# Optimization experiments

Measured on AMD Instinct MI355X. Metric: run time of the kernel, lower is better.

Reference implementation:

```python
import jax, jax.numpy as jnp
import numpy as np
from jax import lax

B, T_IN, T_OUT = 64, 200, 400
D_ENC, D_ARNN, D_DRNN = 512, 1024, 1024
PRENET, ATT_DIM, NFILT, KSIZE, NMEL = 256, 128, 32, 31, 80


def setup_inputs() -> dict:
    key = jax.random.key(0)
    ks = jax.random.split(key, 20)
    sc = lambda k, shape: (jax.random.normal(k, shape, jnp.float32) * 0.02)
    lengths = jnp.maximum(jax.random.randint(ks[0], (B,), 0, T_IN), T_IN // 2)
    return {
        'encoder_outputs': jax.random.normal(ks[1], (B, T_IN, D_ENC), jnp.float32),
        'decoder_inputs': jax.random.normal(ks[2], (T_OUT, B, NMEL), jnp.float32),
        'encoder_outputs_lengths': lengths,
        'W_p1': sc(ks[3], (PRENET, NMEL)),
        'W_p2': sc(ks[4], (PRENET, PRENET)),
        'W_ih_a': sc(ks[5], (4 * D_ARNN, PRENET + D_ENC)),
        'W_hh_a': sc(ks[6], (4 * D_ARNN, D_ARNN)),
        'b_a': jnp.zeros((4 * D_ARNN,), jnp.float32),
        'Wq': sc(ks[7], (ATT_DIM, D_ARNN)),
        'Wmem': sc(ks[8], (ATT_DIM, D_ENC)),
        'v': sc(ks[9], (ATT_DIM,)),
        'Wconv': sc(ks[10], (NFILT, 2, KSIZE)),
        'Wloc': sc(ks[11], (ATT_DIM, NFILT)),
        'W_ih_d': sc(ks[12], (4 * D_DRNN, D_ARNN + D_ENC)),
        'W_hh_d': sc(ks[13], (4 * D_DRNN, D_DRNN)),
        'b_d': jnp.zeros((4 * D_DRNN,), jnp.float32),
        'Wp': sc(ks[14], (NMEL, D_DRNN + D_ENC)),
        'bp': jnp.zeros((NMEL,), jnp.float32),
    }


def _lstm_cell(x, h, c, Wih, Whh, b):
    g = x @ Wih.T + h @ Whh.T + b
    i, f, gg, o = jnp.split(g, 4, axis=-1)
    c_new = jax.nn.sigmoid(f) * c + jax.nn.sigmoid(i) * jnp.tanh(gg)
    h_new = jax.nn.sigmoid(o) * jnp.tanh(c_new)
    return h_new, c_new


def reference(encoder_outputs, decoder_inputs, encoder_outputs_lengths,
              W_p1, W_p2, W_ih_a, W_hh_a, b_a, Wq, Wmem, v, Wconv, Wloc,
              W_ih_d, W_hh_d, b_d, Wp, bp):
    Bsz, T_in, _ = encoder_outputs.shape
    T_steps = decoder_inputs.shape[0]
    NEG = jnp.float32(-1e8)
    pad = (KSIZE - 1) // 2

    # go frame + prenet (prenet_dropout = 0.0 => pure relu MLP)
    go = jnp.zeros((1, Bsz, NMEL), decoder_inputs.dtype)
    di = jnp.concatenate([go, decoder_inputs], axis=0)          # [T+1, B, 80]
    pre = jax.nn.relu(jax.nn.relu(di @ W_p1.T) @ W_p2.T)        # [T+1, B, 256]
    xs = pre[:T_steps]                                          # step i uses pre[i]

    processed_memory = encoder_outputs @ Wmem.T                 # [B, T_in, att]
    mask = jnp.arange(T_in)[None, :] >= encoder_outputs_lengths[:, None]

    def step(carry, x_t):
        ah, ac, dh, dc, aw, aw_cum, actx = carry
        cell_in = jnp.concatenate([x_t, actx], axis=-1)
        ah, ac = _lstm_cell(cell_in, ah, ac, W_ih_a, W_hh_a, b_a)
        # location-sensitive attention
        awc = jnp.stack([aw, aw_cum], axis=1)                   # [B, 2, T_in]
        loc = lax.conv_general_dilated(awc, Wconv, (1,), [(pad, pad)],
                                       dimension_numbers=('NCH', 'OIH', 'NCH'))
        loc = jnp.swapaxes(loc, 1, 2) @ Wloc.T                  # [B, T_in, att]
        pq = (ah @ Wq.T)[:, None, :]                            # [B, 1, att]
        energies = jnp.tanh(pq + loc + processed_memory) @ v    # [B, T_in]
        energies = jnp.where(mask, NEG, energies)
        aw = jax.nn.softmax(energies, axis=1)
        actx = jnp.einsum('bt,bte->be', aw, encoder_outputs)
        aw_cum = aw_cum + aw
        dec_in = jnp.concatenate([ah, actx], axis=-1)
        dh, dc = _lstm_cell(dec_in, dh, dc, W_ih_d, W_hh_d, b_d)
        out = jnp.concatenate([dh, actx], axis=-1) @ Wp.T + bp  # [B, 80]
        return (ah, ac, dh, dc, aw, aw_cum, actx), (out, aw)

    z = lambda d: jnp.zeros((Bsz, d), encoder_outputs.dtype)
    carry0 = (z(D_ARNN), z(D_ARNN), z(D_DRNN), z(D_DRNN), z(T_in), z(T_in), z(D_ENC))
    _, (outs, aligns) = lax.scan(step, carry0, xs)
    return jnp.swapaxes(outs, 0, 1), jnp.swapaxes(aligns, 0, 1)  # [B,T,80], [B,T,T_in]
```

## Files before the change

kernel.cpp:

```cpp
#include <hip/hip_runtime.h>
#include <cstddef>
#include <cstdint>

#define T_INN 200
#define T_OUTT 400
#define BB 64
#define DENC 512
#define NMEL 80

typedef unsigned short u16;
typedef __bf16 bf16x8 __attribute__((ext_vector_type(8)));
typedef float f32x4 __attribute__((ext_vector_type(4)));
typedef float f32x2 __attribute__((ext_vector_type(2)));

__device__ __forceinline__ f32x2 pkfma(f32x2 a, f32x2 b, f32x2 c) {
  return __builtin_elementwise_fma(a, b, c);
}

__device__ __forceinline__ float sigf(float x) {
  return __builtin_amdgcn_rcpf(1.0f + __expf(-x));
}
__device__ __forceinline__ float ftanh(float x) {
  float e2 = __expf(2.0f * x);
  return 1.0f - 2.0f * __builtin_amdgcn_rcpf(e2 + 1.0f);
}

__device__ __forceinline__ u16 f2bf(float f) {
  unsigned u = __float_as_uint(f);
  unsigned r = u + 0x7fffu + ((u >> 16) & 1u);
  return (u16)(r >> 16);
}

__device__ __forceinline__ bf16x8 ldbf8(const u16* p) { return *(const bf16x8*)p; }

__global__ __launch_bounds__(256) void gemm_pre_kernel(
    const float* __restrict__ A, int lda, const float* __restrict__ W, int ldw,
    float* __restrict__ C, u16* __restrict__ Cbf, int ldc, int K, int relu)
{
  __shared__ float As[16][66];
  __shared__ float Ws[16][66];
  const int tid = threadIdx.x;
  const int tn = tid & 15, tm = tid >> 4;
  const int n0 = blockIdx.x * 64;
  const int m0 = blockIdx.y * 64;
  float acc[4][4] = {{0.f}};
  for (int kt = 0; kt < K; kt += 16) {
#pragma unroll
    for (int i = 0; i < 4; i++) {
      int e = tid + 256 * i;
      int m = e >> 4, kk = e & 15;
      As[kk][m] = A[(size_t)(m0 + m) * lda + kt + kk];
    }
#pragma unroll
    for (int i = 0; i < 4; i++) {
      int e = tid + 256 * i;
      int n = e >> 4, kk = e & 15;
      Ws[kk][n] = W[(size_t)(n0 + n) * ldw + kt + kk];
    }
    __syncthreads();
#pragma unroll
    for (int kk = 0; kk < 16; kk++) {
      float2 a01 = *(const float2*)&As[kk][tm * 4];
      float2 a23 = *(const float2*)&As[kk][tm * 4 + 2];
      float2 w01 = *(const float2*)&Ws[kk][tn * 4];
      float2 w23 = *(const float2*)&Ws[kk][tn * 4 + 2];
      float a[4] = {a01.x, a01.y, a23.x, a23.y};
      float w[4] = {w01.x, w01.y, w23.x, w23.y};
#pragma unroll
      for (int mi = 0; mi < 4; mi++)
#pragma unroll
        for (int ni = 0; ni < 4; ni++)
          acc[mi][ni] = fmaf(a[mi], w[ni], acc[mi][ni]);
    }
    __syncthreads();
  }
#pragma unroll
  for (int mi = 0; mi < 4; mi++) {
    int m = m0 + tm * 4 + mi;
    float v0 = acc[mi][0], v1 = acc[mi][1], v2 = acc[mi][2], v3 = acc[mi][3];
    if (relu) {
      v0 = fmaxf(v0, 0.f); v1 = fmaxf(v1, 0.f);
      v2 = fmaxf(v2, 0.f); v3 = fmaxf(v3, 0.f);
    }
    if (Cbf) {
      u16* p = Cbf + (size_t)m * ldc + n0 + tn * 4;
      p[0] = f2bf(v0); p[1] = f2bf(v1); p[2] = f2bf(v2); p[3] = f2bf(v3);
    } else {
      float4 vv; vv.x = v0; vv.y = v1; vv.z = v2; vv.w = v3;
      *(float4*)&C[(size_t)m * ldc + n0 + tn * 4] = vv;
    }
  }
}

__global__ __launch_bounds__(256) void pack_w_kernel(
    const float* __restrict__ W, u16* __restrict__ P,
    int K, int KTl, int ktOff, int KTtot, int total)
{
  int slot = blockIdx.x * 256 + threadIdx.x;
  if (slot >= total) return;
  int lane = slot & 63;
  int ktl = (slot >> 6) % KTl;
  int nt = slot / (64 * KTl);
  int n = nt * 16 + (lane & 15);
  int k = ktl * 32 + (lane >> 4) * 8;
  const float* src = W + (size_t)n * K + k;
  u16 tmp[8];
#pragma unroll
  for (int i = 0; i < 8; i++) tmp[i] = f2bf(src[i]);
  u16* dst = P + ((size_t)(nt * KTtot + (ktl + ktOff)) * 64 + lane) * 8;
  *(uint4*)dst = *(const uint4*)tmp;
}

__global__ void transpose_pm_kernel(const float* __restrict__ pm, float* __restrict__ pmT)
{
  int b = blockIdx.z;
  int tT = blockIdx.x * 32, aT = blockIdx.y * 32;
  __shared__ float tile[32][33];
  int tx = threadIdx.x, ty = threadIdx.y;
#pragma unroll
  for (int i = 0; i < 4; i++) {
    int t = tT + ty + i * 8;
    int a = aT + tx;
    if (t < T_INN) tile[ty + i * 8][tx] = pm[((size_t)b * T_INN + t) * 128 + a];
  }
  __syncthreads();
#pragma unroll
  for (int i = 0; i < 4; i++) {
    int a = aT + ty + i * 8;
    int t = tT + tx;
    if (t < T_INN) pmT[((size_t)b * 128 + a) * T_INN + t] = tile[tx][ty + i * 8];
  }
}

struct SmemGates {
  float part[16][16][66];
  float gred[1024];
};

__global__ __launch_bounds__(1024, 4) void gates_kernel(
    const u16* __restrict__ xs,
    const u16* __restrict__ actx_bf,
    const u16* __restrict__ ah_bf_r, u16* __restrict__ ah_bf_w,
    const u16* __restrict__ dh_bf_r, u16* __restrict__ dh_bf_w,
    const u16* __restrict__ Wa, const u16* __restrict__ Wd,
    const float* __restrict__ b_a, const float* __restrict__ b_d,
    float* __restrict__ ah, float* __restrict__ ac,
    float* __restrict__ dh, float* __restrict__ dc, int t)
{
  const int z = blockIdx.z;
  if (z == 0 && t >= T_OUTT) return;
  if (z == 1 && t < 1) return;
  const int bq = blockIdx.x, ms2 = blockIdx.y;
  const int tid = threadIdx.x;
  const int kw = tid >> 6, lane = tid & 63;
  const int mrow = lane & 15, ksub = (lane >> 4) * 8;
  const int rowL = ms2 * 32 + mrow;
  const int rowH = rowL + 16;
  __shared__ SmemGates sg;

  f32x4 zero4 = {0.f, 0.f, 0.f, 0.f};
  f32x4 aL0 = zero4, aL1 = zero4, aL2 = zero4, aL3 = zero4;
  f32x4 aH0 = zero4, aH1 = zero4, aH2 = zero4, aH3 = zero4;
  const float* bias; float* hF; float* cSt; u16* hw;

  if (z == 0) {
    constexpr int KT = 64;
    const size_t gstride = (size_t)KT * 32768;
    const u16* wb0 = Wa + ((size_t)(bq * KT + kw * 4) * 64 + lane) * 8;
    const u16* rbL; const u16* rbH;
    if (kw < 2) {
      rbL = xs + (size_t)rowL * 256 + ksub + kw * 128;
      rbH = xs + (size_t)rowH * 256 + ksub + kw * 128;
    } else if (kw < 6) {
      rbL = actx_bf + (size_t)rowL * 512 + ksub + kw * 128 - 256;
      rbH = actx_bf + (size_t)rowH * 512 + ksub + kw * 128 - 256;
    } else {
      rbL = ah_bf_r + (size_t)rowL * 1024 + ksub + kw * 128 - 768;
      rbH = ah_bf_r + (size_t)rowH * 1024 + ksub + kw * 128 - 768;
    }
#pragma unroll
    for (int i = 0; i < 4; i++) {
      bf16x8 al = ldbf8(rbL + i * 32);
      bf16x8 ahi = ldbf8(rbH + i * 32);
      const u16* wb = wb0 + (size_t)i * 512;
      bf16x8 w0 = ldbf8(wb);
      bf16x8 w1 = ldbf8(wb + gstride);
      bf16x8 w2 = ldbf8(wb + 2 * gstride);
      bf16x8 w3 = ldbf8(wb + 3 * gstride);
      aL0 = __builtin_amdgcn_mfma_f32_16x16x32_bf16(al, w0, aL0, 0, 0, 0);
      aL1 = __builtin_amdgcn_mfma_f32_16x16x32_bf16(al, w1, aL1, 0, 0, 0);
      aL2 = __builtin_amdgcn_mfma_f32_16x16x32_bf16(al, w2, aL2, 0, 0, 0);
      aL3 = __builtin_amdgcn_mfma_f32_16x16x32_bf16(al, w3, aL3, 0, 0, 0);
      aH0 = __builtin_amdgcn_mfma_f32_16x16x32_bf16(ahi, w0, aH0, 0, 0, 0);
      aH1 = __builtin_amdgcn_mfma_f32_16x16x32_bf16(ahi, w1, aH1, 0, 0, 0);
      aH2 = __builtin_amdgcn_mfma_f32_16x16x32_bf16(ahi, w2, aH2, 0, 0, 0);
      aH3 = __builtin_amdgcn_mfma_f32_16x16x32_bf16(ahi, w3, aH3, 0, 0, 0);
    }
    bias = b_a; hF = ah; cSt = ac; hw = ah_bf_w;
  } else {
    constexpr int KT = 80;
    const size_t gstride = (size_t)KT * 32768;
    const u16* wb0 = Wd + ((size_t)(bq * KT + kw) * 64 + lane) * 8;
    const u16* a0L = ah_bf_r + (size_t)rowL * 1024 + ksub + kw * 32;
    const u16* a1L = actx_bf + (size_t)rowL * 512  + ksub + kw * 32;
    const u16* a2L = dh_bf_r + (size_t)rowL * 1024 + ksub + kw * 32;
    const u16* a0H = ah_bf_r + (size_t)rowH * 1024 + ksub + kw * 32;
    const u16* a1H = actx_bf + (size_t)rowH * 512  + ksub + kw * 32;
    const u16* a2H = dh_bf_r + (size_t)rowH * 1024 + ksub + kw * 32;
#pragma unroll
    for (int i = 0; i < 5; i++) {
      const u16* apL = (i < 2) ? (a0L + i * 512) : ((i == 2) ? a1L : (a2L + (i - 3) * 512));
      const u16* apH = (i < 2) ? (a0H + i * 512) : ((i == 2) ? a1H : (a2H + (i - 3) * 512));
      bf16x8 al = ldbf8(apL);
      bf16x8 ahi = ldbf8(apH);
      const u16* wb = wb0 + (size_t)i * (16 * 512);
      bf16x8 w0 = ldbf8(wb);
      bf16x8 w1 = ldbf8(wb + gstride);
      bf16x8 w2 = ldbf8(wb + 2 * gstride);
      bf16x8 w3 = ldbf8(wb + 3 * gstride);
      aL0 = __builtin_amdgcn_mfma_f32_16x16x32_bf16(al, w0, aL0, 0, 0, 0);
      aL1 = __builtin_amdgcn_mfma_f32_16x16x32_bf16(al, w1, aL1, 0, 0, 0);
      aL2 = __builtin_amdgcn_mfma_f32_16x16x32_bf16(al, w2, aL2, 0, 0, 0);
      aL3 = __builtin_amdgcn_mfma_f32_16x16x32_bf16(al, w3, aL3, 0, 0, 0);
      aH0 = __builtin_amdgcn_mfma_f32_16x16x32_bf16(ahi, w0, aH0, 0, 0, 0);
      aH1 = __builtin_amdgcn_mfma_f32_16x16x32_bf16(ahi, w1, aH1, 0, 0, 0);
      aH2 = __builtin_amdgcn_mfma_f32_16x16x32_bf16(ahi, w2, aH2, 0, 0, 0);
      aH3 = __builtin_amdgcn_mfma_f32_16x16x32_bf16(ahi, w3, aH3, 0, 0, 0);
    }
    bias = b_d; hF = dh; cSt = dc; hw = dh_bf_w;
  }

#pragma unroll
  for (int h = 0; h < 2; h++) {
    if (h == 1) __syncthreads();
#pragma unroll
    for (int r = 0; r < 4; r++) {
      if (h == 0) {
        sg.part[kw][r][lane]      = aL0[r];
        sg.part[kw][4 + r][lane]  = aL1[r];
        sg.part[kw][8 + r][lane]  = aL2[r];
        sg.part[kw][12 + r][lane] = aL3[r];
      } else {
        sg.part[kw][r][lane]      = aH0[r];
        sg.part[kw][4 + r][lane]  = aH1[r];
        sg.part[kw][8 + r][lane]  = aH2[r];
        sg.part[kw][12 + r][lane] = aH3[r];
      }
    }
    __syncthreads();
    {
      int g = tid >> 8, rc = tid & 255, rw = rc >> 4, col = rc & 15;
      int ln = ((rw >> 2) << 4) + col;
      int r = g * 4 + (rw & 3);
      float s = 0.f;
#pragma unroll
      for (int k2 = 0; k2 < 16; k2++) s += sg.part[k2][r][ln];
      sg.gred[tid] = s;
    }
    __syncthreads();
    if (tid < 256) {
      int rw = tid >> 4, col = tid & 15;
      int j = bq * 16 + col, m = ms2 * 32 + h * 16 + rw;
      size_t idx = (size_t)m * 1024 + j;
      float gi = sg.gred[tid]       + bias[j];
      float gf = sg.gred[256 + tid] + bias[j + 1024];
      float gg = sg.gred[512 + tid] + bias[j + 2048];
      float go = sg.gred[768 + tid] + bias[j + 3072];
      float cn = sigf(gf) * cSt[idx] + sigf(gi) * ftanh(gg);
      cSt[idx] = cn;
      float hn = sigf(go) * ftanh(cn);
      hF[idx] = hn;
      hw[idx] = f2bf(hn);
    }
  }
}

__global__ __launch_bounds__(1024, 4) void fused_step_kernel(
    const float* __restrict__ ah, const float* __restrict__ dh,
    float* __restrict__ actx , u16* __restrict__ actx_bf,
    float* __restrict__ aw, float* __restrict__ awcum,
    const float* __restrict__ pmT, const float* __restrict__ Wq,
    const float* __restrict__ Wconv, const float* __restrict__ Wloc,
    const float* __restrict__ vvec, const int* __restrict__ lens,
    const float* __restrict__ enc, const float* __restrict__ Wp,
    const float* __restrict__ bp,
    float* __restrict__ outsOut, float* __restrict__ alignsOut, int t)
{
  const int tid = threadIdx.x;

  if (blockIdx.x >= 64) {
    if (t < 1) return;
    const int bo = blockIdx.x - 64;
    const float* actxR = actx + (size_t)((t - 1) & 1) * 32768;
    __shared__ float cp[1024];
    float s = 0.f;
    int m = tid / 12, sub = tid - m * 12;
    if (tid < 960) {
      const float4* w4 = (const float4*)(Wp + (size_t)m * 1536 + sub * 128);
      const float4* a4 = (sub < 8)
          ? (const float4*)(dh + (size_t)bo * 1024 + sub * 128)
          : (const float4*)(actxR + (size_t)bo * 512 + (sub - 8) * 128);
      f32x2 s2 = {0.f, 0.f};
#pragma unroll 8
      for (int kk = 0; kk < 32; kk++) {
        float4 w = w4[kk], av = a4[kk];
        s2 = pkfma(f32x2{w.x, w.y}, f32x2{av.x, av.y}, s2);
        s2 = pkfma(f32x2{w.z, w.w}, f32x2{av.z, av.w}, s2);
      }
      s = s2.x + s2.y;
    }
    cp[tid] = s;
    __syncthreads();
    if (tid < 80) {
      float acc2 = bp[tid];
#pragma unroll
      for (int i2 = 0; i2 < 12; i2++) acc2 += cp[tid * 12 + i2];
      outsOut[((size_t)bo * T_OUTT + (t - 1)) * NMEL + tid] = acc2;
    }
    return;
  }

  if (t >= T_OUTT) return;
  const int b = blockIdx.x;
  const int g = tid >> 8, ti = tid & 255;
  float* actxW = actx + (size_t)(t & 1) * 32768;

  __shared__ float2 acS[T_INN];
  __shared__ float ahS[1024];
  __shared__ float pp[128][9];
  __shared__ float pqS[128];
  __shared__ float convS[T_INN][33];
  __shared__ float ep[4][256];
  __shared__ float red[256];
  __shared__ float awS[256];
  __shared__ float cpart[1024];

  if (tid < T_INN) {
    float2 v; v.x = aw[b * T_INN + tid]; v.y = awcum[b * T_INN + tid];
    acS[tid] = v;
  }
  ahS[tid] = ah[(size_t)b * 1024 + tid];
  __syncthreads();
  {
    int a = tid >> 3, kc = tid & 7;
    const float4* wv = (const float4*)(Wq + (size_t)a * 1024 + kc * 128);
    const float4* hv = (const float4*)(ahS + kc * 128);
    f32x2 s2 = {0.f, 0.f};
#pragma unroll 8
    for (int i = 0; i < 32; i++) {
      float4 wq = wv[i], hh = hv[i];
      s2 = pkfma(f32x2{wq.x, wq.y}, f32x2{hh.x, hh.y}, s2);
      s2 = pkfma(f32x2{wq.z, wq.w}, f32x2{hh.z, hh.w}, s2);
    }
    pp[a][kc] = s2.x + s2.y;
  }
  __syncthreads();
  if (tid < 128) {
    float s = 0.f;
#pragma unroll
    for (int kc = 0; kc < 8; kc++) s += pp[tid][kc];
    pqS[tid] = s;
  }
  if (ti < T_INN) {
    f32x2 s2[4] = {{0.f, 0.f}, {0.f, 0.f}, {0.f, 0.f}, {0.f, 0.f}};
#pragma unroll
    for (int k = 0; k < 31; k++) {
      int tt = ti + k - 15;
      if (tt >= 0 && tt < T_INN) {
        float2 v = acS[tt];
        f32x2 vx = {v.x, v.x}, vy = {v.y, v.y};
#pragma unroll
        for (int p = 0; p < 4; p++) {
          int f = g * 8 + 2 * p;
          f32x2 wa = {Wconv[f * 62 + k],      Wconv[(f + 1) * 62 + k]};
          f32x2 wc = {Wconv[f * 62 + 31 + k], Wconv[(f + 1) * 62 + 31 + k]};
          s2[p] = pkfma(wa, vx, s2[p]);
          s2[p] = pkfma(wc, vy, s2[p]);
        }
      }
    }
#pragma unroll
    for (int p = 0; p < 4; p++) {
      convS[ti][g * 8 + 2 * p]     = s2[p].x;
      convS[ti][g * 8 + 2 * p + 1] = s2[p].y;
    }
  }
  __syncthreads();
  float e = 0.f;
  if (ti < T_INN) {
    float cv[32];
#pragma unroll
    for (int f = 0; f < 32; f++) cv[f] = convS[ti][f];
    const float* pm = pmT + ((size_t)b * 128 + g * 32) * T_INN + ti;
#pragma unroll 4
    for (int aa = 0; aa < 32; aa++) {
      int a = g * 32 + aa;
      const float* wl = Wloc + a * 32;
      f32x2 x2 = {0.f, 0.f};
#pragma unroll
      for (int j = 0; j < 16; j++) {
        f32x2 w2 = *(const f32x2*)&wl[2 * j];
        x2 = pkfma(w2, f32x2{cv[2 * j], cv[2 * j + 1]}, x2);
      }
      float x = pqS[a] + pm[(size_t)aa * T_INN] + x2.x + x2.y;
      float ex2 = __expf(2.f * x);
      e += vvec[a] * (1.f - 2.f * __builtin_amdgcn_rcpf(ex2 + 1.f));
    }
  }
  ep[g][ti] = e;
  __syncthreads();
  float ev = -3.0e38f, ex = 0.f;
  if (tid < 256) {
    if (tid < T_INN) {
      ev = ep[0][tid] + ep[1][tid] + ep[2][tid] + ep[3][tid];
      if (tid >= lens[b]) ev = -100000000.0f;
    }
    red[tid] = ev;
  }
  __syncthreads();
  for (int s2 = 128; s2 > 0; s2 >>= 1) {
    if (tid < s2) red[tid] = fmaxf(red[tid], red[tid + s2]);
    __syncthreads();
  }
  float mx = red[0];
  __syncthreads();
  if (tid < 256) { ex = (tid < T_INN) ? __expf(ev - mx) : 0.f; red[tid] = ex; }
  __syncthreads();
  for (int s2 = 128; s2 > 0; s2 >>= 1) {
    if (tid < s2) red[tid] += red[tid + s2];
    __syncthreads();
  }
  float inv = 1.0f / red[0];
  if (tid < T_INN) {
    float a = ex * inv;
    awS[tid] = a;
    aw[b * T_INN + tid] = a;
    awcum[b * T_INN + tid] = acS[tid].y + a;
    alignsOut[((size_t)b * T_OUTT + t) * T_INN + tid] = a;
  }
  __syncthreads();
  {
    int e0 = tid & 511, half = tid >> 9;
    const float* ep2 = enc + ((size_t)b * T_INN + half * 100) * DENC + e0;
    float s = 0.f;
#pragma unroll 4
    for (int tt = 0; tt < 100; tt++) s += awS[half * 100 + tt] * ep2[(size_t)tt * DENC];
    cpart[tid] = s;
  }
  __syncthreads();
  if (tid < 512) {
    float v2 = cpart[tid] + cpart[512 + tid];
    actxW[b * DENC + tid] = v2;
    actx_bf[b * DENC + tid] = f2bf(v2);
  }
}

extern "C" void kernel_launch(void* const* d_in, const int* in_sizes, int n_in,
                              void* d_out, int out_size, void* d_ws, size_t ws_size,
                              hipStream_t stream)
{
  const float* enc    = (const float*)d_in[0];
  const float* dec    = (const float*)d_in[1];
  const int*   lens   = (const int*)d_in[2];
  const float* W_p1   = (const float*)d_in[3];
  const float* W_p2   = (const float*)d_in[4];
  const float* W_ih_a = (const float*)d_in[5];
  const float* W_hh_a = (const float*)d_in[6];
  const float* b_a    = (const float*)d_in[7];
  const float* Wq     = (const float*)d_in[8];
  const float* Wmem   = (const float*)d_in[9];
  const float* vvec   = (const float*)d_in[10];
  const float* Wconv  = (const float*)d_in[11];
  const float* Wloc   = (const float*)d_in[12];
  const float* W_ih_d = (const float*)d_in[13];
  const float* W_hh_d = (const float*)d_in[14];
  const float* b_d    = (const float*)d_in[15];
  const float* Wp     = (const float*)d_in[16];
  const float* bp     = (const float*)d_in[17];

  float* ws = (float*)d_ws;
  size_t off = 0;
  u16* xs_bf = (u16*)(ws + off); off += (size_t)T_OUTT * 64 * 256 / 2;
  float* pmT = ws + off; off += (size_t)64 * 128 * T_INN;
  u16* Wa_pack = (u16*)(ws + off); off += (size_t)4096 * 2048 / 2;
  u16* Wd_pack = (u16*)(ws + off); off += (size_t)4096 * 2560 / 2;
  float* stateBase = ws + off;
  float* ah    = stateBase;
  float* dh    = ah + 65536;
  float* ac    = dh + 65536;
  float* dc    = ac + 65536;
  float* actx  = dc + 65536;
  float* aw    = actx + 2 * 32768;
  float* awcum = aw + 12800;
  u16* ah_bf   = (u16*)(awcum + 12800);
  u16* dh_bf   = ah_bf + 2 * 65536;
  u16* actx_bf = dh_bf + 2 * 65536;
  size_t stateFloats = 4 * 65536 + 2 * 32768 + 2 * 12800
                     + (2 * 65536 + 2 * 65536 + 32768) / 2;
  off += stateFloats;
  float* scratch = ws + off;
  float* h1 = scratch;
  float* pmt = scratch;

  float* outsOut   = (float*)d_out;
  float* alignsOut = outsOut + (size_t)BB * T_OUTT * NMEL;

  hipMemsetAsync(stateBase, 0, stateFloats * sizeof(float), stream);
  hipMemsetAsync(xs_bf, 0, (size_t)64 * 256 * sizeof(u16), stream);
  hipMemsetAsync(Wa_pack, 0, (size_t)4096 * 2048 * sizeof(u16), stream);

  {
    int tot;
    tot = 256 * 24 * 64;
    pack_w_kernel<<<(tot + 255) / 256, 256, 0, stream>>>(W_ih_a, Wa_pack, 768, 24, 0, 64, tot);
    tot = 256 * 32 * 64;
    pack_w_kernel<<<(tot + 255) / 256, 256, 0, stream>>>(W_hh_a, Wa_pack, 1024, 32, 24, 64, tot);
    tot = 256 * 48 * 64;
    pack_w_kernel<<<(tot + 255) / 256, 256, 0, stream>>>(W_ih_d, Wd_pack, 1536, 48, 0, 80, tot);
    tot = 256 * 32 * 64;
    pack_w_kernel<<<(tot + 255) / 256, 256, 0, stream>>>(W_hh_d, Wd_pack, 1024, 32, 48, 80, tot);
  }
  gemm_pre_kernel<<<dim3(4, 399), 256, 0, stream>>>(dec, 80, W_p1, 80, h1, nullptr, 256, 80, 1);
  gemm_pre_kernel<<<dim3(4, 399), 256, 0, stream>>>(h1, 256, W_p2, 256, nullptr, xs_bf + 64 * 256, 256, 256, 1);
  gemm_pre_kernel<<<dim3(2, 200), 256, 0, stream>>>(enc, 512, Wmem, 512, pmt, nullptr, 128, 512, 0);
  transpose_pm_kernel<<<dim3(7, 4, 64), dim3(32, 8), 0, stream>>>(pmt, pmT);

  for (int t = 0; t <= T_OUTT; t++) {
    int tc = (t < T_OUTT) ? t : 0;
    gates_kernel<<<dim3(64, 2, 2), 1024, 0, stream>>>(
        xs_bf + (size_t)tc * 64 * 256,
        actx_bf,
        ah_bf + (size_t)((t + 1) & 1) * 65536, ah_bf + (size_t)(t & 1) * 65536,
        dh_bf + (size_t)(t & 1) * 65536,       dh_bf + (size_t)((t + 1) & 1) * 65536,
        Wa_pack, Wd_pack, b_a, b_d, ah, ac, dh, dc, t);
    fused_step_kernel<<<128, 1024, 0, stream>>>(
        ah, dh, actx, actx_bf, aw, awcum, pmT, Wq, Wconv, Wloc, vvec,
        lens, enc, Wp, bp, outsOut, alignsOut, t);
  }
}
```

Baseline: 33.92 ms.

## Re-pipeline decoder step: overlap attention with decoder LSTM and projection with attention LSTM

Restructures the per-step kernel schedule so the decoder LSTM gates (for the previous step) run in the same launch as the attention computation, and the output projection runs alongside the attention-LSTM gates, delaying outputs by one extra step. Triple-buffers actx and double-buffers dh so the skewed stages read consistent state, and adds one extra loop iteration to drain the pipeline. Also replaces the shared-memory tree reductions in softmax with wavefront shuffle reductions. The aim is fewer serialized dependencies and better use of CUs per step, at the cost of more buffer-indexing complexity.

```diff
diff --git a/kernel.cpp b/kernel.cpp
--- a/kernel.cpp
+++ b/kernel.cpp
@@ -136,37 +136,41 @@
   float part[16][16][66];
   float gred[1024];
 };
-
-__global__ __launch_bounds__(1024, 4) void gates_kernel(
-    const u16* __restrict__ xs,
-    const u16* __restrict__ actx_bf,
-    const u16* __restrict__ ah_bf_r, u16* __restrict__ ah_bf_w,
-    const u16* __restrict__ dh_bf_r, u16* __restrict__ dh_bf_w,
-    const u16* __restrict__ Wa, const u16* __restrict__ Wd,
-    const float* __restrict__ b_a, const float* __restrict__ b_d,
-    float* __restrict__ ah, float* __restrict__ ac,
-    float* __restrict__ dh, float* __restrict__ dc, int t)
-{
-  const int z = blockIdx.z;
-  if (z == 0 && t >= T_OUTT) return;
-  if (z == 1 && t < 1) return;
-  const int bq = blockIdx.x, ms2 = blockIdx.y;
-  const int tid = threadIdx.x;
+struct SmemAtt {
+  float2 acS[T_INN];
+  float ahS[1024];
+  float pp[128][9];
+  float pqS[128];
+  float convS[T_INN][33];
+  float ep[4][256];
+  float red[256];
+  float awS[256];
+  float cpart[1024];
+};
+union SmemU { SmemGates g; SmemAtt a; };
+
+template <int Z>
+__device__ __forceinline__ void gates_body(
+    const u16* __restrict__ xs, const u16* __restrict__ actx_bf,
+    const u16* __restrict__ h1_bf, const u16* __restrict__ h2_bf,
+    const u16* __restrict__ Wpack,
+    const float* __restrict__ bias,
+    float* __restrict__ hF, float* __restrict__ cSt, u16* __restrict__ hw,
+    int bq, int ms2, int tid, SmemGates& sg)
+{
   const int kw = tid >> 6, lane = tid & 63;
   const int mrow = lane & 15, ksub = (lane >> 4) * 8;
   const int rowL = ms2 * 32 + mrow;
   const int rowH = rowL + 16;
-  __shared__ SmemGates sg;
 
   f32x4 zero4 = {0.f, 0.f, 0.f, 0.f};
   f32x4 aL0 = zero4, aL1 = zero4, aL2 = zero4, aL3 = zero4;
   f32x4 aH0 = zero4, aH1 = zero4, aH2 = zero4, aH3 = zero4;
-  const float* bias; float* hF; float* cSt; u16* hw;
-
-  if (z == 0) {
+
+  if constexpr (Z == 0) {
     constexpr int KT = 64;
     const size_t gstride = (size_t)KT * 32768;
-    const u16* wb0 = Wa + ((size_t)(bq * KT + kw * 4) * 64 + lane) * 8;
+    const u16* wb0 = Wpack + ((size_t)(bq * KT + kw * 4) * 64 + lane) * 8;
     const u16* rbL; const u16* rbH;
     if (kw < 2) {
       rbL = xs + (size_t)rowL * 256 + ksub + kw * 128;
@@ -175,8 +179,8 @@
       rbL = actx_bf + (size_t)rowL * 512 + ksub + kw * 128 - 256;
       rbH = actx_bf + (size_t)rowH * 512 + ksub + kw * 128 - 256;
     } else {
-      rbL = ah_bf_r + (size_t)rowL * 1024 + ksub + kw * 128 - 768;
-      rbH = ah_bf_r + (size_t)rowH * 1024 + ksub + kw * 128 - 768;
+      rbL = h1_bf + (size_t)rowL * 1024 + ksub + kw * 128 - 768;
+      rbH = h1_bf + (size_t)rowH * 1024 + ksub + kw * 128 - 768;
     }
 #pragma unroll
     for (int i = 0; i < 4; i++) {
@@ -196,17 +200,16 @@
       aH2 = __builtin_amdgcn_mfma_f32_16x16x32_bf16(ahi, w2, aH2, 0, 0, 0);
       aH3 = __builtin_amdgcn_mfma_f32_16x16x32_bf16(ahi, w3, aH3, 0, 0, 0);
     }
-    bias = b_a; hF = ah; cSt = ac; hw = ah_bf_w;
   } else {
     constexpr int KT = 80;
     const size_t gstride = (size_t)KT * 32768;
-    const u16* wb0 = Wd + ((size_t)(bq * KT + kw) * 64 + lane) * 8;
-    const u16* a0L = ah_bf_r + (size_t)rowL * 1024 + ksub + kw * 32;
+    const u16* wb0 = Wpack + ((size_t)(bq * KT + kw) * 64 + lane) * 8;
+    const u16* a0L = h1_bf   + (size_t)rowL * 1024 + ksub + kw * 32;
     const u16* a1L = actx_bf + (size_t)rowL * 512  + ksub + kw * 32;
-    const u16* a2L = dh_bf_r + (size_t)rowL * 1024 + ksub + kw * 32;
-    const u16* a0H = ah_bf_r + (size_t)rowH * 1024 + ksub + kw * 32;
+    const u16* a2L = h2_bf   + (size_t)rowL * 1024 + ksub + kw * 32;
+    const u16* a0H = h1_bf   + (size_t)rowH * 1024 + ksub + kw * 32;
     const u16* a1H = actx_bf + (size_t)rowH * 512  + ksub + kw * 32;
-    const u16* a2H = dh_bf_r + (size_t)rowH * 1024 + ksub + kw * 32;
+    const u16* a2H = h2_bf   + (size_t)rowH * 1024 + ksub + kw * 32;
 #pragma unroll
     for (int i = 0; i < 5; i++) {
       const u16* apL = (i < 2) ? (a0L + i * 512) : ((i == 2) ? a1L : (a2L + (i - 3) * 512));
@@ -227,7 +230,6 @@
       aH2 = __builtin_amdgcn_mfma_f32_16x16x32_bf16(ahi, w2, aH2, 0, 0, 0);
       aH3 = __builtin_amdgcn_mfma_f32_16x16x32_bf16(ahi, w3, aH3, 0, 0, 0);
     }
-    bias = b_d; hF = dh; cSt = dc; hw = dh_bf_w;
   }
 
 #pragma unroll
@@ -275,31 +277,30 @@
   }
 }
 
-__global__ __launch_bounds__(1024, 4) void fused_step_kernel(
-    const float* __restrict__ ah, const float* __restrict__ dh,
-    float* __restrict__ actx , u16* __restrict__ actx_bf,
-    float* __restrict__ aw, float* __restrict__ awcum,
-    const float* __restrict__ pmT, const float* __restrict__ Wq,
-    const float* __restrict__ Wconv, const float* __restrict__ Wloc,
-    const float* __restrict__ vvec, const int* __restrict__ lens,
-    const float* __restrict__ enc, const float* __restrict__ Wp,
-    const float* __restrict__ bp,
-    float* __restrict__ outsOut, float* __restrict__ alignsOut, int t)
+__global__ __launch_bounds__(1024, 4) void stepA_kernel(
+    const u16* __restrict__ xs, const u16* __restrict__ actx_bf_r,
+    const u16* __restrict__ ah_bf_r, u16* __restrict__ ah_bf_w,
+    const u16* __restrict__ Wa, const float* __restrict__ b_a,
+    float* __restrict__ ah, float* __restrict__ ac,
+    const float* __restrict__ dh_r,
+    const float* __restrict__ actx_r,
+    const float* __restrict__ Wp, const float* __restrict__ bp,
+    float* __restrict__ outsOut, int t)
 {
   const int tid = threadIdx.x;
-
-  if (blockIdx.x >= 64) {
-    if (t < 1) return;
-    const int bo = blockIdx.x - 64;
-    const float* actxR = actx + (size_t)((t - 1) & 1) * 32768;
-    __shared__ float cp[1024];
+  __shared__ SmemGates sg;
+
+  if (blockIdx.x >= 128) {
+    if (t < 2) return;
+    const int bo = blockIdx.x - 128;
+    float* cp = sg.gred;
     float s = 0.f;
     int m = tid / 12, sub = tid - m * 12;
     if (tid < 960) {
       const float4* w4 = (const float4*)(Wp + (size_t)m * 1536 + sub * 128);
       const float4* a4 = (sub < 8)
-          ? (const float4*)(dh + (size_t)bo * 1024 + sub * 128)
-          : (const float4*)(actxR + (size_t)bo * 512 + (sub - 8) * 128);
+          ? (const float4*)(dh_r + (size_t)bo * 1024 + sub * 128)
+          : (const float4*)(actx_r + (size_t)bo * 512 + (sub - 8) * 128);
       f32x2 s2 = {0.f, 0.f};
 #pragma unroll 8
       for (int kk = 0; kk < 32; kk++) {
@@ -315,36 +316,55 @@
       float acc2 = bp[tid];
 #pragma unroll
       for (int i2 = 0; i2 < 12; i2++) acc2 += cp[tid * 12 + i2];
-      outsOut[((size_t)bo * T_OUTT + (t - 1)) * NMEL + tid] = acc2;
-    }
+      outsOut[((size_t)bo * T_OUTT + (t - 2)) * NMEL + tid] = acc2;
+    }
+    return;
+  }
+  if (t >= T_OUTT) return;
+  gates_body<0>(xs, actx_bf_r, ah_bf_r, nullptr, Wa, b_a, ah, ac, ah_bf_w,
+                blockIdx.x & 63, blockIdx.x >> 6, tid, sg);
+}
+
+__global__ __launch_bounds__(1024, 4) void stepB_kernel(
+    const float* __restrict__ ah,
+    float* __restrict__ actx_w, u16* __restrict__ actx_bf_w,
+    float* __restrict__ aw, float* __restrict__ awcum,
+    const float* __restrict__ pmT, const float* __restrict__ Wq,
+    const float* __restrict__ Wconv, const float* __restrict__ Wloc,
+    const float* __restrict__ vvec, const int* __restrict__ lens,
+    const float* __restrict__ enc, float* __restrict__ alignsOut,
+    const u16* __restrict__ ah_bf_r, const u16* __restrict__ actx_bf_r,
+    const u16* __restrict__ dh_bf_r, u16* __restrict__ dh_bf_w,
+    float* __restrict__ dh_w,
+    const u16* __restrict__ Wd, const float* __restrict__ b_d,
+    float* __restrict__ dc, int t)
+{
+  const int tid = threadIdx.x;
+  __shared__ SmemU sm;
+
+  if (blockIdx.x >= 64) {
+    if (t < 1 || t > T_OUTT) return;
+    const int bb = blockIdx.x - 64;
+    gates_body<1>(nullptr, actx_bf_r, ah_bf_r, dh_bf_r, Wd, b_d,
+                  dh_w, dc, dh_bf_w, bb & 63, bb >> 6, tid, sm.g);
     return;
   }
 
   if (t >= T_OUTT) return;
   const int b = blockIdx.x;
   const int g = tid >> 8, ti = tid & 255;
-  float* actxW = actx + (size_t)(t & 1) * 32768;
-
-  __shared__ float2 acS[T_INN];
-  __shared__ float ahS[1024];
-  __shared__ float pp[128][9];
-  __shared__ float pqS[128];
-  __shared__ float convS[T_INN][33];
-  __shared__ float ep[4][256];
-  __shared__ float red[256];
-  __shared__ float awS[256];
-  __shared__ float cpart[1024];
+  SmemAtt& sa = sm.a;
 
   if (tid < T_INN) {
     float2 v; v.x = aw[b * T_INN + tid]; v.y = awcum[b * T_INN + tid];
-    acS[tid] = v;
-  }
-  ahS[tid] = ah[(size_t)b * 1024 + tid];
+    sa.acS[tid] = v;
+  }
+  sa.ahS[tid] = ah[(size_t)b * 1024 + tid];
   __syncthreads();
   {
     int a = tid >> 3, kc = tid & 7;
     const float4* wv = (const float4*)(Wq + (size_t)a * 1024 + kc * 128);
-    const float4* hv = (const float4*)(ahS + kc * 128);
+    const float4* hv = (const float4*)(sa.ahS + kc * 128);
     f32x2 s2 = {0.f, 0.f};
 #pragma unroll 8
     for (int i = 0; i < 32; i++) {
@@ -352,14 +372,14 @@
       s2 = pkfma(f32x2{wq.x, wq.y}, f32x2{hh.x, hh.y}, s2);
       s2 = pkfma(f32x2{wq.z, wq.w}, f32x2{hh.z, hh.w}, s2);
     }
-    pp[a][kc] = s2.x + s2.y;
+    sa.pp[a][kc] = s2.x + s2.y;
   }
   __syncthreads();
   if (tid < 128) {
     float s = 0.f;
 #pragma unroll
-    for (int kc = 0; kc < 8; kc++) s += pp[tid][kc];
-    pqS[tid] = s;
+    for (int kc = 0; kc < 8; kc++) s += sa.pp[tid][kc];
+    sa.pqS[tid] = s;
   }
   if (ti < T_INN) {
     f32x2 s2[4] = {{0.f, 0.f}, {0.f, 0.f}, {0.f, 0.f}, {0.f, 0.f}};
@@ -367,7 +387,7 @@
     for (int k = 0; k < 31; k++) {
       int tt = ti + k - 15;
       if (tt >= 0 && tt < T_INN) {
-        float2 v = acS[tt];
+        float2 v = sa.acS[tt];
         f32x2 vx = {v.x, v.x}, vy = {v.y, v.y};
 #pragma unroll
         for (int p = 0; p < 4; p++) {
@@ -381,8 +401,8 @@
     }
 #pragma unroll
     for (int p = 0; p < 4; p++) {
-      convS[ti][g * 8 + 2 * p]     = s2[p].x;
-      convS[ti][g * 8 + 2 * p + 1] = s2[p].y;
+      sa.convS[ti][g * 8 + 2 * p]     = s2[p].x;
+      sa.convS[ti][g * 8 + 2 * p + 1] = s2[p].y;
     }
   }
   __syncthreads();
@@ -390,7 +410,7 @@
   if (ti < T_INN) {
     float cv[32];
 #pragma unroll
-    for (int f = 0; f < 32; f++) cv[f] = convS[ti][f];
+    for (int f = 0; f < 32; f++) cv[f] = sa.convS[ti][f];
     const float* pm = pmT + ((size_t)b * 128 + g * 32) * T_INN + ti;
 #pragma unroll 4
     for (int aa = 0; aa < 32; aa++) {
@@ -402,40 +422,38 @@
         f32x2 w2 = *(const f32x2*)&wl[2 * j];
         x2 = pkfma(w2, f32x2{cv[2 * j], cv[2 * j + 1]}, x2);
       }
-      float x = pqS[a] + pm[(size_t)aa * T_INN] + x2.x + x2.y;
+      float x = sa.pqS[a] + pm[(size_t)aa * T_INN] + x2.x + x2.y;
       float ex2 = __expf(2.f * x);
       e += vvec[a] * (1.f - 2.f * __builtin_amdgcn_rcpf(ex2 + 1.f));
     }
   }
-  ep[g][ti] = e;
-  __syncthreads();
-  float ev = -3.0e38f, ex = 0.f;
+  sa.ep[g][ti] = e;
+  __syncthreads();
+  float ev = -3.0e38f;
   if (tid < 256) {
     if (tid < T_INN) {
-      ev = ep[0][tid] + ep[1][tid] + ep[2][tid] + ep[3][tid];
+      ev = sa.ep[0][tid] + sa.ep[1][tid] + sa.ep[2][tid] + sa.ep[3][tid];
       if (tid >= lens[b]) ev = -100000000.0f;
     }
-    red[tid] = ev;
-  }
-  __syncthreads();
-  for (int s2 = 128; s2 > 0; s2 >>= 1) {
-    if (tid < s2) red[tid] = fmaxf(red[tid], red[tid + s2]);
-    __syncthreads();
-  }
-  float mx = red[0];
-  __syncthreads();
-  if (tid < 256) { ex = (tid < T_INN) ? __expf(ev - mx) : 0.f; red[tid] = ex; }
-  __syncthreads();
-  for (int s2 = 128; s2 > 0; s2 >>= 1) {
-    if (tid < s2) red[tid] += red[tid + s2];
-    __syncthreads();
-  }
-  float inv = 1.0f / red[0];
+  }
+  float mloc = ev;
+#pragma unroll
+  for (int o = 32; o > 0; o >>= 1) mloc = fmaxf(mloc, __shfl_xor(mloc, o));
+  if (tid < 256 && (tid & 63) == 0) sa.red[tid >> 6] = mloc;
+  __syncthreads();
+  float mx = fmaxf(fmaxf(sa.red[0], sa.red[1]), fmaxf(sa.red[2], sa.red[3]));
+  float ex = (tid < T_INN) ? __expf(ev - mx) : 0.f;
+  float sloc = ex;
+#pragma unroll
+  for (int o = 32; o > 0; o >>= 1) sloc += __shfl_xor(sloc, o);
+  if (tid < 256 && (tid & 63) == 0) sa.red[4 + (tid >> 6)] = sloc;
+  __syncthreads();
+  float inv = 1.0f / ((sa.red[4] + sa.red[5]) + (sa.red[6] + sa.red[7]));
   if (tid < T_INN) {
     float a = ex * inv;
-    awS[tid] = a;
+    sa.awS[tid] = a;
     aw[b * T_INN + tid] = a;
-    awcum[b * T_INN + tid] = acS[tid].y + a;
+    awcum[b * T_INN + tid] = sa.acS[tid].y + a;
     alignsOut[((size_t)b * T_OUTT + t) * T_INN + tid] = a;
   }
   __syncthreads();
@@ -444,14 +462,14 @@
     const float* ep2 = enc + ((size_t)b * T_INN + half * 100) * DENC + e0;
     float s = 0.f;
 #pragma unroll 4
-    for (int tt = 0; tt < 100; tt++) s += awS[half * 100 + tt] * ep2[(size_t)tt * DENC];
-    cpart[tid] = s;
+    for (int tt = 0; tt < 100; tt++) s += sa.awS[half * 100 + tt] * ep2[(size_t)tt * DENC];
+    sa.cpart[tid] = s;
   }
   __syncthreads();
   if (tid < 512) {
-    float v2 = cpart[tid] + cpart[512 + tid];
-    actxW[b * DENC + tid] = v2;
-    actx_bf[b * DENC + tid] = f2bf(v2);
+    float v2 = sa.cpart[tid] + sa.cpart[512 + tid];
+    actx_w[b * DENC + tid] = v2;
+    actx_bf_w[b * DENC + tid] = f2bf(v2);
   }
 }
 
@@ -487,16 +505,16 @@
   float* stateBase = ws + off;
   float* ah    = stateBase;
   float* dh    = ah + 65536;
-  float* ac    = dh + 65536;
+  float* ac    = dh + 2 * 65536;
   float* dc    = ac + 65536;
   float* actx  = dc + 65536;
-  float* aw    = actx + 2 * 32768;
+  float* aw    = actx + 3 * 32768;
   float* awcum = aw + 12800;
   u16* ah_bf   = (u16*)(awcum + 12800);
   u16* dh_bf   = ah_bf + 2 * 65536;
   u16* actx_bf = dh_bf + 2 * 65536;
-  size_t stateFloats = 4 * 65536 + 2 * 32768 + 2 * 12800
-                     + (2 * 65536 + 2 * 65536 + 32768) / 2;
+  size_t stateFloats = 65536 + 2 * 65536 + 65536 + 65536 + 3 * 32768 + 2 * 12800
+                     + (2 * 65536 + 2 * 65536 + 3 * 32768) / 2;
   off += stateFloats;
   float* scratch = ws + off;
   float* h1 = scratch;
@@ -525,16 +543,30 @@
   gemm_pre_kernel<<<dim3(2, 200), 256, 0, stream>>>(enc, 512, Wmem, 512, pmt, nullptr, 128, 512, 0);
   transpose_pm_kernel<<<dim3(7, 4, 64), dim3(32, 8), 0, stream>>>(pmt, pmT);
 
-  for (int t = 0; t <= T_OUTT; t++) {
+  for (int t = 0; t <= T_OUTT + 1; t++) {
     int tc = (t < T_OUTT) ? t : 0;
-    gates_kernel<<<dim3(64, 2, 2), 1024, 0, stream>>>(
+    int sW = t % 3;
+    int sA = (t + 2) % 3;
+    int sO = (t + 1) % 3;
+    stepA_kernel<<<192, 1024, 0, stream>>>(
         xs_bf + (size_t)tc * 64 * 256,
-        actx_bf,
-        ah_bf + (size_t)((t + 1) & 1) * 65536, ah_bf + (size_t)(t & 1) * 65536,
-        dh_bf + (size_t)(t & 1) * 65536,       dh_bf + (size_t)((t + 1) & 1) * 65536,
-        Wa_pack, Wd_pack, b_a, b_d, ah, ac, dh, dc, t);
-    fused_step_kernel<<<128, 1024, 0, stream>>>(
-        ah, dh, actx, actx_bf, aw, awcum, pmT, Wq, Wconv, Wloc, vvec,
-        lens, enc, Wp, bp, outsOut, alignsOut, t);
-  }
-}
+        actx_bf + (size_t)sA * 32768,
+        ah_bf + (size_t)((t + 1) & 1) * 65536,
+        ah_bf + (size_t)(t & 1) * 65536,
+        Wa_pack, b_a, ah, ac,
+        dh + (size_t)(t & 1) * 65536,
+        actx + (size_t)sO * 32768,
+        Wp, bp, outsOut, t);
+    if (t <= T_OUTT)
+      stepB_kernel<<<192, 1024, 0, stream>>>(
+          ah,
+          actx + (size_t)sW * 32768, actx_bf + (size_t)sW * 32768,
+          aw, awcum, pmT, Wq, Wconv, Wloc, vvec, lens, enc, alignsOut,
+          ah_bf + (size_t)((t + 1) & 1) * 65536,
+          actx_bf + (size_t)sA * 32768,
+          dh_bf + (size_t)(t & 1) * 65536,
+          dh_bf + (size_t)((t + 1) & 1) * 65536,
+          dh + (size_t)((t + 1) & 1) * 65536,
+          Wd_pack, b_d, dc, t);
+  }
+}
```

After: 40.03 ms. 18.0% more time.
